# Performance work log

Hardware: AMD Instinct MI355X
Metric: run time of the kernel (lower is better)

Reference implementation:

```python
import jax, jax.numpy as jnp
import numpy as np

N, E, G = 50000, 800000, 128
IN_C, H, EDGE_D, NUM_CLASSES, NUM_LAYERS = 26, 64, 3, 2, 4

def _p(k, shape):
    return jax.random.normal(k, shape, dtype=jnp.float32) * 0.05

def setup_inputs() -> dict:
    key = jax.random.key(0)
    ks = list(jax.random.split(key, 32))
    x = jax.random.normal(ks[0], (N, IN_C), dtype=jnp.float32)
    pos = jax.random.normal(ks[1], (N, 3), dtype=jnp.float32)
    row = jax.random.randint(ks[2], (E,), 0, N, dtype=jnp.int32)
    # avoid self-loops so dist > 0 (norm is non-differentiable at 0)
    off = jax.random.randint(ks[3], (E,), 1, N, dtype=jnp.int32)
    col = (row + off) % N
    edge_index = jnp.stack([row, col], axis=0)
    edge_attr = jax.random.normal(ks[4], (E, EDGE_D), dtype=jnp.float32)
    batch = jnp.sort(jax.random.randint(ks[5], (N,), 0, G, dtype=jnp.int32))
    inp = dict(x=x, pos=pos, edge_index=edge_index, edge_attr=edge_attr, batch=batch)
    inp['proj_W'] = _p(ks[6], (IN_C, H)); inp['proj_b'] = jnp.zeros((H,), jnp.float32)
    inp['msg_W1'] = _p(ks[7], (NUM_LAYERS, 2*H + 1 + EDGE_D, H)); inp['msg_b1'] = jnp.zeros((NUM_LAYERS, H), jnp.float32)
    inp['msg_W2'] = _p(ks[8], (NUM_LAYERS, H, H)); inp['msg_b2'] = jnp.zeros((NUM_LAYERS, H), jnp.float32)
    inp['node_W1'] = _p(ks[9], (NUM_LAYERS, 2*H, H)); inp['node_b1'] = jnp.zeros((NUM_LAYERS, H), jnp.float32)
    inp['node_W2'] = _p(ks[10], (NUM_LAYERS, H, H)); inp['node_b2'] = jnp.zeros((NUM_LAYERS, H), jnp.float32)
    inp['coord_W1'] = _p(ks[11], (NUM_LAYERS - 1, H, H)); inp['coord_b1'] = jnp.zeros((NUM_LAYERS - 1, H), jnp.float32)
    inp['coord_W2'] = _p(ks[12], (NUM_LAYERS - 1, H, 1)); inp['coord_b2'] = jnp.zeros((NUM_LAYERS - 1, 1), jnp.float32)
    inp['cls_W1'] = _p(ks[13], (2*H, H)); inp['cls_b1'] = jnp.zeros((H,), jnp.float32)
    inp['cls_W2'] = _p(ks[14], (H, NUM_CLASSES)); inp['cls_b2'] = jnp.zeros((NUM_CLASSES,), jnp.float32)
    return inp

def _egnn_forward(x, pos, edge_index, edge_attr, batch,
                  proj_W, proj_b, msg_W1, msg_b1, msg_W2, msg_b2,
                  node_W1, node_b1, node_W2, node_b2,
                  coord_W1, coord_b1, coord_W2, coord_b2,
                  cls_W1, cls_b1, cls_W2, cls_b2):
    silu = jax.nn.silu
    row, col = edge_index[0], edge_index[1]
    h = x @ proj_W + proj_b  # [N,H]
    for i in range(NUM_LAYERS):
        diff = pos[row] - pos[col]                      # [E,3]
        dist = jnp.linalg.norm(diff, axis=-1, keepdims=True)  # [E,1]
        msg_in = jnp.concatenate([h[row], h[col], dist, edge_attr], axis=-1)  # [E,2H+1+edge_dim]
        msg = silu(silu(msg_in @ msg_W1[i] + msg_b1[i]) @ msg_W2[i] + msg_b2[i])  # [E,H]
        agg = jax.ops.segment_sum(msg, row, num_segments=N)  # [N,H]
        h_new = silu(jnp.concatenate([h, agg], axis=-1) @ node_W1[i] + node_b1[i]) @ node_W2[i] + node_b2[i]
        h = h + h_new  # residual; dropout is identity at eval
        if i < NUM_LAYERS - 1:
            w = silu(msg @ coord_W1[i] + coord_b1[i]) @ coord_W2[i] + coord_b2[i]  # [E,1]
            pos = pos + jax.ops.segment_sum(diff * w, row, num_segments=N)
    # mean_max pooling over graphs
    sums = jax.ops.segment_sum(h, batch, num_segments=G)
    counts = jax.ops.segment_sum(jnp.ones((h.shape[0],), h.dtype), batch, num_segments=G)
    mean = sums / jnp.maximum(counts, 1.0)[:, None]
    mx = jax.ops.segment_max(h, batch, num_segments=G)
    pooled = jnp.concatenate([mean, mx], axis=-1)  # [G,2H]
    return jax.nn.relu(pooled @ cls_W1 + cls_b1) @ cls_W2 + cls_b2  # [G,num_classes]

def reference(x, pos, edge_index, edge_attr, batch,
              proj_W, proj_b, msg_W1, msg_b1, msg_W2, msg_b2,
              node_W1, node_b1, node_W2, node_b2,
              coord_W1, coord_b1, coord_W2, coord_b2,
              cls_W1, cls_b1, cls_W2, cls_b2):
    return _egnn_forward(x, pos, edge_index, edge_attr, batch,
                         proj_W, proj_b, msg_W1, msg_b1, msg_W2, msg_b2,
                         node_W1, node_b1, node_W2, node_b2,
                         coord_W1, coord_b1, coord_W2, coord_b2,
                         cls_W1, cls_b1, cls_W2, cls_b2)
```

## Files before the change

### kernel.cpp

```cpp
#include <hip/hip_runtime.h>
#include <math.h>


typedef __attribute__((ext_vector_type(8))) short bshort8;
typedef __attribute__((ext_vector_type(4))) float f32x4;
typedef unsigned short ushort;
typedef unsigned int uint;

__device__ __forceinline__ float silu_f(float x)
{
  return x * __builtin_amdgcn_rcpf(1.0f + __expf(-x));
}

__device__ __forceinline__ void bf16_split(float x, ushort& h, ushort& l)
{
  uint bx = __float_as_uint(x);
  ushort hb = (ushort)(bx >> 16);
  float hf = __uint_as_float((uint)hb << 16);
  float r = x - hf;
  l = (ushort)(__float_as_uint(r) >> 16);
  h = hb;
}

#define ROW_FMA(acc, scal, rowptr)                                                   \
  {                                                                                  \
    const float4* _w = (const float4*)(rowptr);                                      \
    _Pragma("unroll") for (int _j = 0; _j < 16; _j++)                                \
    {                                                                                \
      float4 _wv = _w[_j];                                                           \
      acc[4 * _j + 0] += (scal) * _wv.x;                                             \
      acc[4 * _j + 1] += (scal) * _wv.y;                                             \
      acc[4 * _j + 2] += (scal) * _wv.z;                                             \
      acc[4 * _j + 3] += (scal) * _wv.w;                                             \
    }                                                                                \
  }

__global__ __launch_bounds__(256) void proj_kernel(
    const float* __restrict__ x, const float* __restrict__ W, const float* __restrict__ b,
    float* __restrict__ h, int N)
{
  __shared__ float sW[26 * 64];
  __shared__ float sb[64];
  for (int i = threadIdx.x; i < 26 * 64; i += 256) sW[i] = W[i];
  if (threadIdx.x < 64) sb[threadIdx.x] = b[threadIdx.x];
  __syncthreads();
  int n = blockIdx.x * 256 + threadIdx.x;
  if (n >= N) return;
  float acc[64];
#pragma unroll
  for (int j = 0; j < 64; j++) acc[j] = sb[j];
#pragma unroll
  for (int k = 0; k < 26; k++) {
    float xk = x[(size_t)n * 26 + k];
    ROW_FMA(acc, xk, sW + k * 64);
  }
  float4* h4 = (float4*)(h + (size_t)n * 64);
#pragma unroll
  for (int j4 = 0; j4 < 16; j4++) {
    float4 v;
    v.x = acc[4 * j4 + 0]; v.y = acc[4 * j4 + 1]; v.z = acc[4 * j4 + 2]; v.w = acc[4 * j4 + 3];
    h4[j4] = v;
  }
}

#define EB 128

__device__ __forceinline__ bshort8 lds_frag(const ushort* base, int edge, int kb)
{
  int byte = edge * 128 + kb * 2;
  byte ^= (edge & 7) << 4;
  return *(const bshort8*)((const char*)base + byte);
}

__device__ __forceinline__ void stage_tile_f32(
    const float* __restrict__ src, int n0, int N, ushort* sHi, ushort* sLo, int t)
{
#pragma unroll
  for (int p = 0; p < 4; p++) {
    int nl = p * 32 + (t >> 3);
    int ks = t & 7;
    int n = n0 + nl;
    int base = nl * 128 + ks * 16;
    int swz = (nl & 7) << 4;
    if (n < N) {
      const float4* sp = (const float4*)(src + (size_t)n * 64) + ks * 2;
      float4 a0 = sp[0], a1 = sp[1];
      float va[8] = {a0.x, a0.y, a0.z, a0.w, a1.x, a1.y, a1.z, a1.w};
      ushort hh[8], ll[8];
#pragma unroll
      for (int kk = 0; kk < 8; kk++) bf16_split(va[kk], hh[kk], ll[kk]);
      uint4 hv, lv;
      hv.x = (uint)hh[0] | ((uint)hh[1] << 16);
      hv.y = (uint)hh[2] | ((uint)hh[3] << 16);
      hv.z = (uint)hh[4] | ((uint)hh[5] << 16);
      hv.w = (uint)hh[6] | ((uint)hh[7] << 16);
      lv.x = (uint)ll[0] | ((uint)ll[1] << 16);
      lv.y = (uint)ll[2] | ((uint)ll[3] << 16);
      lv.z = (uint)ll[4] | ((uint)ll[5] << 16);
      lv.w = (uint)ll[6] | ((uint)ll[7] << 16);
      *(uint4*)((char*)sHi + (base ^ swz)) = hv;
      *(uint4*)((char*)sLo + (base ^ swz)) = lv;
    } else {
      uint4 z; z.x = 0; z.y = 0; z.z = 0; z.w = 0;
      *(uint4*)((char*)sHi + (base ^ swz)) = z;
      *(uint4*)((char*)sLo + (base ^ swz)) = z;
    }
  }
}

#define PANEL_MFMA(accv, bhp, blp, sHi, sLo)                                         \
  {                                                                                  \
    bshort8 wh0 = *(const bshort8*)(bhp);                                            \
    bshort8 wh1 = *(const bshort8*)((bhp) + 32);                                     \
    bshort8 wl0 = *(const bshort8*)(blp);                                            \
    bshort8 wl1 = *(const bshort8*)((blp) + 32);                                     \
    _Pragma("unroll") for (int et = 0; et < 8; et++)                                 \
    {                                                                                \
      int nd = et * 16 + lane16;                                                     \
      bshort8 ah0 = lds_frag(sHi, nd, kq * 8);                                       \
      bshort8 ah1 = lds_frag(sHi, nd, 32 + kq * 8);                                  \
      bshort8 al0 = lds_frag(sLo, nd, kq * 8);                                       \
      bshort8 al1 = lds_frag(sLo, nd, 32 + kq * 8);                                  \
      f32x4 a = accv[et];                                                            \
      a = __builtin_amdgcn_mfma_f32_16x16x32_bf16(wh0, ah0, a, 0, 0, 0);             \
      a = __builtin_amdgcn_mfma_f32_16x16x32_bf16(wh1, ah1, a, 0, 0, 0);             \
      a = __builtin_amdgcn_mfma_f32_16x16x32_bf16(wh0, al0, a, 0, 0, 0);             \
      a = __builtin_amdgcn_mfma_f32_16x16x32_bf16(wh1, al1, a, 0, 0, 0);             \
      a = __builtin_amdgcn_mfma_f32_16x16x32_bf16(wl0, ah0, a, 0, 0, 0);             \
      a = __builtin_amdgcn_mfma_f32_16x16x32_bf16(wl1, ah1, a, 0, 0, 0);             \
      accv[et] = a;                                                                  \
    }                                                                                \
  }

__global__ __launch_bounds__(256) void premul_mfma_kernel(
    const float* __restrict__ h, const ushort* __restrict__ pqh, const ushort* __restrict__ pql,
    float* __restrict__ P, float* __restrict__ Q, int N)
{
  __shared__ ushort sAhi[EB * 64];
  __shared__ ushort sAlo[EB * 64];
  int t = threadIdx.x;
  int n0 = blockIdx.x * EB;
  stage_tile_f32(h, n0, N, sAhi, sAlo, t);
  __syncthreads();

  int l = t & 63, wv = t >> 6, lane16 = l & 15, kq = l >> 4;
  int col = wv * 16 + kq * 4;

  f32x4 acc[8];
#pragma unroll
  for (int et = 0; et < 8; et++) { f32x4 z = {0.f, 0.f, 0.f, 0.f}; acc[et] = z; }
  {
    const ushort* bh = pqh + (wv * 16 + lane16) * 64 + kq * 8;
    const ushort* bl = pql + (wv * 16 + lane16) * 64 + kq * 8;
    PANEL_MFMA(acc, bh, bl, sAhi, sAlo);
  }
#pragma unroll
  for (int et = 0; et < 8; et++) {
    int n = n0 + et * 16 + lane16;
    if (n < N) {
      float4 v; v.x = acc[et][0]; v.y = acc[et][1]; v.z = acc[et][2]; v.w = acc[et][3];
      *(float4*)(P + (size_t)n * 64 + col) = v;
    }
  }
#pragma unroll
  for (int et = 0; et < 8; et++) { f32x4 z = {0.f, 0.f, 0.f, 0.f}; acc[et] = z; }
  {
    const ushort* bh = pqh + 4096 + (wv * 16 + lane16) * 64 + kq * 8;
    const ushort* bl = pql + 4096 + (wv * 16 + lane16) * 64 + kq * 8;
    PANEL_MFMA(acc, bh, bl, sAhi, sAlo);
  }
#pragma unroll
  for (int et = 0; et < 8; et++) {
    int n = n0 + et * 16 + lane16;
    if (n < N) {
      float4 v; v.x = acc[et][0]; v.y = acc[et][1]; v.z = acc[et][2]; v.w = acc[et][3];
      *(float4*)(Q + (size_t)n * 64 + col) = v;
    }
  }
}

template <int PREMUL>
__global__ __launch_bounds__(256) void node_mfma_kernel(
    float* __restrict__ h, const float* __restrict__ agg,
    const ushort* __restrict__ n1h, const ushort* __restrict__ n1l,
    const float* __restrict__ b1,
    const ushort* __restrict__ n2h, const ushort* __restrict__ n2l,
    const float* __restrict__ b2,
    const ushort* __restrict__ pqh, const ushort* __restrict__ pql,
    float* __restrict__ P, float* __restrict__ Q, int N)
{
  __shared__ ushort sAhi[EB * 64];
  __shared__ ushort sAlo[EB * 64];
  __shared__ float sb1v[64], sb2v[64];
  int t = threadIdx.x;
  int n0 = blockIdx.x * EB;
  if (t < 64) { sb1v[t] = b1[t]; sb2v[t] = b2[t]; }

  stage_tile_f32(h, n0, N, sAhi, sAlo, t);
  __syncthreads();

  int l = t & 63, wv = t >> 6, lane16 = l & 15, kq = l >> 4;
  int col = wv * 16 + kq * 4;

  f32x4 acc[8];
#pragma unroll
  for (int et = 0; et < 8; et++) { f32x4 z = {0.f, 0.f, 0.f, 0.f}; acc[et] = z; }
  {
    const ushort* bh = n1h + (wv * 16 + lane16) * 128 + kq * 8;
    const ushort* bl = n1l + (wv * 16 + lane16) * 128 + kq * 8;
    PANEL_MFMA(acc, bh, bl, sAhi, sAlo);
  }
  __syncthreads();
  stage_tile_f32(agg, n0, N, sAhi, sAlo, t);
  __syncthreads();
  {
    const ushort* bh = n1h + (wv * 16 + lane16) * 128 + 64 + kq * 8;
    const ushort* bl = n1l + (wv * 16 + lane16) * 128 + 64 + kq * 8;
    PANEL_MFMA(acc, bh, bl, sAhi, sAlo);
  }
  __syncthreads();

  {
    float b1r[4];
#pragma unroll
    for (int r = 0; r < 4; r++) b1r[r] = sb1v[col + r];
#pragma unroll
    for (int et = 0; et < 8; et++) {
      int nd = et * 16 + lane16;
      ushort uh[4], ul[4];
#pragma unroll
      for (int r = 0; r < 4; r++) {
        float uv = silu_f(acc[et][r] + b1r[r]);
        bf16_split(uv, uh[r], ul[r]);
      }
      int byte = (nd * 128 + col * 2) ^ ((nd & 7) << 4);
      uint2 hv, lv;
      hv.x = (uint)uh[0] | ((uint)uh[1] << 16);
      hv.y = (uint)uh[2] | ((uint)uh[3] << 16);
      lv.x = (uint)ul[0] | ((uint)ul[1] << 16);
      lv.y = (uint)ul[2] | ((uint)ul[3] << 16);
      *(uint2*)((char*)sAhi + byte) = hv;
      *(uint2*)((char*)sAlo + byte) = lv;
    }
  }
  __syncthreads();

#pragma unroll
  for (int et = 0; et < 8; et++) { f32x4 z = {0.f, 0.f, 0.f, 0.f}; acc[et] = z; }
  {
    const ushort* bh = n2h + (wv * 16 + lane16) * 64 + kq * 8;
    const ushort* bl = n2l + (wv * 16 + lane16) * 64 + kq * 8;
    PANEL_MFMA(acc, bh, bl, sAhi, sAlo);
  }
  uint2 hnh[8], hnl[8];
  {
    float b2r[4];
#pragma unroll
    for (int r = 0; r < 4; r++) b2r[r] = sb2v[col + r];
#pragma unroll
    for (int et = 0; et < 8; et++) {
      int n = n0 + et * 16 + lane16;
      float hn[4];
      if (n < N) {
        float4 hv = *(float4*)(h + (size_t)n * 64 + col);
        hn[0] = hv.x + acc[et][0] + b2r[0];
        hn[1] = hv.y + acc[et][1] + b2r[1];
        hn[2] = hv.z + acc[et][2] + b2r[2];
        hn[3] = hv.w + acc[et][3] + b2r[3];
        float4 sv; sv.x = hn[0]; sv.y = hn[1]; sv.z = hn[2]; sv.w = hn[3];
        *(float4*)(h + (size_t)n * 64 + col) = sv;
      } else {
        hn[0] = hn[1] = hn[2] = hn[3] = 0.f;
      }
      if (PREMUL) {
        ushort sh[4], sl[4];
#pragma unroll
        for (int r = 0; r < 4; r++) bf16_split(hn[r], sh[r], sl[r]);
        hnh[et].x = (uint)sh[0] | ((uint)sh[1] << 16);
        hnh[et].y = (uint)sh[2] | ((uint)sh[3] << 16);
        hnl[et].x = (uint)sl[0] | ((uint)sl[1] << 16);
        hnl[et].y = (uint)sl[2] | ((uint)sl[3] << 16);
      }
    }
  }

  if (PREMUL) {
    __syncthreads();
#pragma unroll
    for (int et = 0; et < 8; et++) {
      int nd = et * 16 + lane16;
      int byte = (nd * 128 + col * 2) ^ ((nd & 7) << 4);
      *(uint2*)((char*)sAhi + byte) = hnh[et];
      *(uint2*)((char*)sAlo + byte) = hnl[et];
    }
    __syncthreads();
#pragma unroll
    for (int et = 0; et < 8; et++) { f32x4 z = {0.f, 0.f, 0.f, 0.f}; acc[et] = z; }
    {
      const ushort* bh = pqh + (wv * 16 + lane16) * 64 + kq * 8;
      const ushort* bl = pql + (wv * 16 + lane16) * 64 + kq * 8;
      PANEL_MFMA(acc, bh, bl, sAhi, sAlo);
    }
#pragma unroll
    for (int et = 0; et < 8; et++) {
      int n = n0 + et * 16 + lane16;
      if (n < N) {
        float4 v; v.x = acc[et][0]; v.y = acc[et][1]; v.z = acc[et][2]; v.w = acc[et][3];
        *(float4*)(P + (size_t)n * 64 + col) = v;
      }
    }
#pragma unroll
    for (int et = 0; et < 8; et++) { f32x4 z = {0.f, 0.f, 0.f, 0.f}; acc[et] = z; }
    {
      const ushort* bh = pqh + 4096 + (wv * 16 + lane16) * 64 + kq * 8;
      const ushort* bl = pql + 4096 + (wv * 16 + lane16) * 64 + kq * 8;
      PANEL_MFMA(acc, bh, bl, sAhi, sAlo);
    }
#pragma unroll
    for (int et = 0; et < 8; et++) {
      int n = n0 + et * 16 + lane16;
      if (n < N) {
        float4 v; v.x = acc[et][0]; v.y = acc[et][1]; v.z = acc[et][2]; v.w = acc[et][3];
        *(float4*)(Q + (size_t)n * 64 + col) = v;
      }
    }
  }
}

__global__ __launch_bounds__(256) void hist_kernel(
    const int* __restrict__ row, int* __restrict__ cnt, int E)
{
  int e = blockIdx.x * 256 + threadIdx.x;
  if (e < E) atomicAdd(&cnt[row[e]], 1);
}

__global__ __launch_bounds__(1024) void scan_kernel(
    const int* __restrict__ cnt, int* __restrict__ rowptr, int* __restrict__ cursor, int N, int E)
{
  __shared__ int part[1024];
  int t = threadIdx.x;
  int chunk = (N + 1023) >> 10;
  int lo = t * chunk;
  int hi = lo + chunk;
  if (lo > N) lo = N;
  if (hi > N) hi = N;
  int s = 0;
  for (int i = lo; i < hi; i++) s += cnt[i];
  part[t] = s;
  __syncthreads();
  for (int off = 1; off < 1024; off <<= 1) {
    int v = 0;
    if (t >= off) v = part[t - off];
    __syncthreads();
    if (t >= off) part[t] += v;
    __syncthreads();
  }
  int run = part[t] - s;
  for (int i = lo; i < hi; i++) {
    rowptr[i] = run;
    cursor[i] = run;
    run += cnt[i];
  }
  if (t == 0) rowptr[N] = E;
}

__global__ __launch_bounds__(256) void scatter_kernel(
    const int* __restrict__ row, const int* __restrict__ col, const float* __restrict__ eattr,
    int* __restrict__ cursor, int* __restrict__ srow, int* __restrict__ scol,
    float* __restrict__ sea4, int E)
{
  int e = blockIdx.x * 256 + threadIdx.x;
  if (e >= E) return;
  int r = row[e];
  int p = atomicAdd(&cursor[r], 1);
  srow[p] = r;
  scol[p] = col[e];
  float4 v;
  v.x = eattr[(size_t)e * 3 + 0];
  v.y = eattr[(size_t)e * 3 + 1];
  v.z = eattr[(size_t)e * 3 + 2];
  v.w = 0.f;
  ((float4*)sea4)[p] = v;
}

__global__ __launch_bounds__(256) void prep_wt_kernel(
    const float* __restrict__ W2all, const float* __restrict__ C1all,
    ushort* __restrict__ w2h, ushort* __restrict__ w2l,
    ushort* __restrict__ c1h, ushort* __restrict__ c1l)
{
  int idx = blockIdx.x * 256 + threadIdx.x;
  if (idx >= 4 * 4096) return;
  int layer = idx >> 12, rem = idx & 4095;
  int k = rem >> 6, c = rem & 63;
  int oidx = layer * 4096 + c * 64 + k;
  ushort h, l;
  bf16_split(W2all[idx], h, l);
  w2h[oidx] = h; w2l[oidx] = l;
  if (layer < 3) {
    bf16_split(C1all[idx], h, l);
    c1h[oidx] = h; c1l[oidx] = l;
  }
}

__global__ __launch_bounds__(256) void prep_nd_kernel(
    const float* __restrict__ ndW1, const float* __restrict__ ndW2,
    const float* __restrict__ msgW1,
    ushort* __restrict__ n1h, ushort* __restrict__ n1l,
    ushort* __restrict__ n2h, ushort* __restrict__ n2l,
    ushort* __restrict__ pqh, ushort* __restrict__ pql)
{
  int idx = blockIdx.x * 256 + threadIdx.x;
  if (idx < 4 * 8192) {
    int i = idx >> 13, rem = idx & 8191;
    int k = rem >> 6, c = rem & 63;
    ushort h, l;
    bf16_split(ndW1[idx], h, l);
    int o = i * 8192 + c * 128 + k;
    n1h[o] = h; n1l[o] = l;
  }
  if (idx < 4 * 4096) {
    int i = idx >> 12, rem = idx & 4095;
    int k = rem >> 6, c = rem & 63;
    ushort h, l;
    bf16_split(ndW2[idx], h, l);
    int o = i * 4096 + c * 64 + k;
    n2h[o] = h; n2l[o] = l;
  }
  if (idx < 4 * 8192) {
    int i = idx >> 13, rem = idx & 8191;
    int k = rem >> 6, c = rem & 63;
    ushort h, l;
    bf16_split(msgW1[(size_t)i * 132 * 64 + k * 64 + c], h, l);
    int o = i * 8192 + (k >> 6) * 4096 + c * 64 + (k & 63);
    pqh[o] = h; pql[o] = l;
  }
}

template <int COORD>
__global__ __launch_bounds__(256) void edge_fused_kernel(
    const int* __restrict__ srow, const int* __restrict__ scol, const int* __restrict__ rowptr,
    const float* __restrict__ posr, float* __restrict__ posw,
    const float* __restrict__ sea4,
    const float* __restrict__ P, const float* __restrict__ Q,
    const float* __restrict__ W1t, const float* __restrict__ b1,
    const ushort* __restrict__ w2h, const ushort* __restrict__ w2l,
    const float* __restrict__ b2,
    const ushort* __restrict__ c1h, const ushort* __restrict__ c1l,
    const float* __restrict__ cb1, const float* __restrict__ cW2,
    const float* __restrict__ cb2,
    float* __restrict__ agg, int E)
{
  __shared__ ushort sUhi[EB * 64];
  __shared__ ushort sUlo[EB * 64];
  __shared__ float sW1t[4 * 64];
  __shared__ float sb1v[64], sb2v[64];
  __shared__ float sDiff[3][EB];
  __shared__ float sWe[EB];
  __shared__ int sShare[COORD ? EB * 4 : EB];
  __shared__ float scb1v[COORD ? 64 : 1];
  __shared__ float scW2v[COORD ? 64 : 1];
  __shared__ int sSlotCnt[2];
  __shared__ int sSlotStart[EB + 2];
  __shared__ int sSlotRowF[EB];

  int* s_srow = sShare;
  float* sPart = (float*)sShare;

  int t = threadIdx.x;
  sW1t[t] = W1t[t];
  if (t < 64) { sb1v[t] = b1[t]; sb2v[t] = b2[t]; }
  if (COORD && t >= 64 && t < 128) { scb1v[t - 64] = cb1[t - 64]; scW2v[t - 64] = cW2[t - 64]; }
  __syncthreads();

  int e0 = blockIdx.x * EB;
  int nE = E - e0; if (nE > EB) nE = EB;

#pragma unroll
  for (int p = 0; p < 4; p++) {
    int eloc = p * 32 + (t >> 3);
    int ks = t & 7;
    int e = e0 + eloc;
    int base = eloc * 128 + ks * 16;
    int swz = (eloc & 7) << 4;
    if (e < E) {
      int r = srow[e];
      int c = scol[e];
      float prx = posr[(size_t)r * 3 + 0], pry = posr[(size_t)r * 3 + 1],
            prz = posr[(size_t)r * 3 + 2];
      float pcx = posr[(size_t)c * 3 + 0], pcy = posr[(size_t)c * 3 + 1],
            pcz = posr[(size_t)c * 3 + 2];
      float dx = prx - pcx, dy = pry - pcy, dz = prz - pcz;
      float dist = sqrtf(dx * dx + dy * dy + dz * dz);
      if (ks == 0) {
        s_srow[eloc] = r;
        sDiff[0][eloc] = dx; sDiff[1][eloc] = dy; sDiff[2][eloc] = dz;
      }
      float4 ea = ((const float4*)sea4)[e];
      const float4* P4p = (const float4*)(P + (size_t)r * 64) + ks * 2;
      const float4* Q4p = (const float4*)(Q + (size_t)c * 64) + ks * 2;
      float4 a0 = P4p[0], a1 = P4p[1];
      float4 q0 = Q4p[0], q1 = Q4p[1];
      float pa[8] = {a0.x, a0.y, a0.z, a0.w, a1.x, a1.y, a1.z, a1.w};
      float qa[8] = {q0.x, q0.y, q0.z, q0.w, q1.x, q1.y, q1.z, q1.w};
      ushort hh[8], ll[8];
#pragma unroll
      for (int kk = 0; kk < 8; kk++) {
        int k = ks * 8 + kk;
        float val = pa[kk] + qa[kk] + sb1v[k] + dist * sW1t[k] + ea.x * sW1t[64 + k] +
                    ea.y * sW1t[128 + k] + ea.z * sW1t[192 + k];
        float uv = silu_f(val);
        bf16_split(uv, hh[kk], ll[kk]);
      }
      uint4 hv, lv;
      hv.x = (uint)hh[0] | ((uint)hh[1] << 16);
      hv.y = (uint)hh[2] | ((uint)hh[3] << 16);
      hv.z = (uint)hh[4] | ((uint)hh[5] << 16);
      hv.w = (uint)hh[6] | ((uint)hh[7] << 16);
      lv.x = (uint)ll[0] | ((uint)ll[1] << 16);
      lv.y = (uint)ll[2] | ((uint)ll[3] << 16);
      lv.z = (uint)ll[4] | ((uint)ll[5] << 16);
      lv.w = (uint)ll[6] | ((uint)ll[7] << 16);
      *(uint4*)((char*)sUhi + (base ^ swz)) = hv;
      *(uint4*)((char*)sUlo + (base ^ swz)) = lv;
    } else {
      uint4 z; z.x = 0; z.y = 0; z.z = 0; z.w = 0;
      *(uint4*)((char*)sUhi + (base ^ swz)) = z;
      *(uint4*)((char*)sUlo + (base ^ swz)) = z;
    }
  }
  __syncthreads();

  bool isstart = false;
  int pre = 0;
  if (t < 128) {
    int le = t;
    isstart = (le < nE) && (le == 0 || s_srow[le] != s_srow[le - 1]);
    unsigned long long m = __ballot(isstart ? 1 : 0);
    int lane = t & 63;
    pre = __popcll(m & ((lane == 0) ? 0ull : ((~0ull) >> (64 - lane))));
    if (lane == 0) sSlotCnt[t >> 6] = __popcll(m);
  }
  __syncthreads();
  if (t < 128 && isstart) {
    int le = t;
    int slot = ((t >> 6) ? sSlotCnt[0] : 0) + pre;
    int row = s_srow[le];
    sSlotStart[slot] = le;
    int rs = rowptr[row], re = rowptr[row + 1];
    int interior = (rs >= e0 && re <= e0 + nE) ? 1 : 0;
    sSlotRowF[slot] = row | (interior << 30);
  }
  if (t == 0) sSlotStart[sSlotCnt[0] + sSlotCnt[1]] = nE;

  int l = t & 63;
  int wv = t >> 6;
  int lane16 = l & 15;
  int kq = l >> 4;

  {
    const ushort* bhp = w2h + (wv * 16 + lane16) * 64 + kq * 8;
    const ushort* blp = w2l + (wv * 16 + lane16) * 64 + kq * 8;
    bshort8 wh0 = *(const bshort8*)(bhp);
    bshort8 wh1 = *(const bshort8*)(bhp + 32);
    bshort8 wl0 = *(const bshort8*)(blp);
    bshort8 wl1 = *(const bshort8*)(blp + 32);

    f32x4 acc[8];
#pragma unroll
    for (int et = 0; et < 8; et++) {
      int edge = et * 16 + lane16;
      bshort8 uh0 = lds_frag(sUhi, edge, kq * 8);
      bshort8 uh1 = lds_frag(sUhi, edge, 32 + kq * 8);
      bshort8 ul0 = lds_frag(sUlo, edge, kq * 8);
      bshort8 ul1 = lds_frag(sUlo, edge, 32 + kq * 8);
      f32x4 a = {0.f, 0.f, 0.f, 0.f};
      a = __builtin_amdgcn_mfma_f32_16x16x32_bf16(wh0, uh0, a, 0, 0, 0);
      a = __builtin_amdgcn_mfma_f32_16x16x32_bf16(wh1, uh1, a, 0, 0, 0);
      a = __builtin_amdgcn_mfma_f32_16x16x32_bf16(wh0, ul0, a, 0, 0, 0);
      a = __builtin_amdgcn_mfma_f32_16x16x32_bf16(wh1, ul1, a, 0, 0, 0);
      a = __builtin_amdgcn_mfma_f32_16x16x32_bf16(wl0, uh0, a, 0, 0, 0);
      a = __builtin_amdgcn_mfma_f32_16x16x32_bf16(wl1, uh1, a, 0, 0, 0);
      acc[et] = a;
    }
    __syncthreads();

    float b2r[4];
#pragma unroll
    for (int r = 0; r < 4; r++) b2r[r] = sb2v[wv * 16 + kq * 4 + r];
#pragma unroll
    for (int et = 0; et < 8; et++) {
      int edge = et * 16 + lane16;
      ushort mh[4], ml[4];
#pragma unroll
      for (int r = 0; r < 4; r++) {
        float mv = silu_f(acc[et][r] + b2r[r]);
        bf16_split(mv, mh[r], ml[r]);
      }
      int byte = (edge * 128 + (wv * 16 + kq * 4) * 2) ^ ((edge & 7) << 4);
      uint2 hv, lv;
      hv.x = (uint)mh[0] | ((uint)mh[1] << 16);
      hv.y = (uint)mh[2] | ((uint)mh[3] << 16);
      lv.x = (uint)ml[0] | ((uint)ml[1] << 16);
      lv.y = (uint)ml[2] | ((uint)ml[3] << 16);
      *(uint2*)((char*)sUhi + byte) = hv;
      *(uint2*)((char*)sUlo + byte) = lv;
    }
  }
  __syncthreads();

  if (COORD) {
    const ushort* chp = c1h + (wv * 16 + lane16) * 64 + kq * 8;
    const ushort* clp = c1l + (wv * 16 + lane16) * 64 + kq * 8;
    bshort8 ch0 = *(const bshort8*)(chp);
    bshort8 ch1 = *(const bshort8*)(chp + 32);
    bshort8 cl0 = *(const bshort8*)(clp);
    bshort8 cl1 = *(const bshort8*)(clp + 32);
    float cb1r[4], cw2r[4];
#pragma unroll
    for (int r = 0; r < 4; r++) {
      cb1r[r] = scb1v[wv * 16 + kq * 4 + r];
      cw2r[r] = scW2v[wv * 16 + kq * 4 + r];
    }
#pragma unroll
    for (int et = 0; et < 8; et++) {
      int edge = et * 16 + lane16;
      bshort8 mh0 = lds_frag(sUhi, edge, kq * 8);
      bshort8 mh1 = lds_frag(sUhi, edge, 32 + kq * 8);
      f32x4 a = {0.f, 0.f, 0.f, 0.f};
      a = __builtin_amdgcn_mfma_f32_16x16x32_bf16(ch0, mh0, a, 0, 0, 0);
      a = __builtin_amdgcn_mfma_f32_16x16x32_bf16(ch1, mh1, a, 0, 0, 0);
      a = __builtin_amdgcn_mfma_f32_16x16x32_bf16(cl0, mh0, a, 0, 0, 0);
      a = __builtin_amdgcn_mfma_f32_16x16x32_bf16(cl1, mh1, a, 0, 0, 0);
      float pr = 0.f;
#pragma unroll
      for (int r = 0; r < 4; r++) pr += silu_f(a[r] + cb1r[r]) * cw2r[r];
      pr += __shfl_xor(pr, 16);
      pr += __shfl_xor(pr, 32);
      if (kq == 0) sPart[edge * 4 + wv] = pr;
    }
  }
  __syncthreads();
  if (COORD) {
    if (t >= 128) {
      int e = t - 128;
      sWe[e] = sPart[4 * e + 0] + sPart[4 * e + 1] + sPart[4 * e + 2] + sPart[4 * e + 3] + cb2[0];
    }
  }
  __syncthreads();

  int nslots = sSlotCnt[0] + sSlotCnt[1];
  for (int task = t; task < (nslots << 5); task += 256) {
    int s = task >> 5, cp = task & 31;
    int a = sSlotStart[s], b = sSlotStart[s + 1];
    float acc0 = 0.f, acc1 = 0.f;
    for (int le = a; le < b; le++) {
      int byte = (le * 128 + cp * 4) ^ ((le & 7) << 4);
      uint hv = *(const uint*)((const char*)sUhi + byte);
      uint lv = *(const uint*)((const char*)sUlo + byte);
      acc0 += __uint_as_float(hv << 16) + __uint_as_float(lv << 16);
      acc1 += __uint_as_float(hv & 0xffff0000u) + __uint_as_float(lv & 0xffff0000u);
    }
    int rowf = sSlotRowF[s];
    int row = rowf & 0x3fffffff;
    float* ap = agg + (size_t)row * 64 + 2 * cp;
    if (rowf & (1 << 30)) {
      ap[0] = acc0; ap[1] = acc1;
    } else {
      atomicAdd(ap, acc0);
      atomicAdd(ap + 1, acc1);
    }
  }
  if (COORD) {
    for (int task = t; task < (nslots << 2); task += 256) {
      int s = task >> 2, d = task & 3;
      if (d < 3) {
        int a = sSlotStart[s], b = sSlotStart[s + 1];
        float acc = 0.f;
        for (int le = a; le < b; le++) acc += sDiff[d][le] * sWe[le];
        int row = sSlotRowF[s] & 0x3fffffff;
        atomicAdd(&posw[(size_t)row * 3 + d], acc);
      }
    }
  }
}

__device__ __forceinline__ int lbound(const int* __restrict__ a, int n, int v)
{
  int lo = 0, hi = n;
  while (lo < hi) {
    int mid = (lo + hi) >> 1;
    if (a[mid] < v) lo = mid + 1;
    else hi = mid;
  }
  return lo;
}

__global__ __launch_bounds__(256) void pool_cls_kernel(
    const float* __restrict__ h, const int* __restrict__ batch, int N,
    const float* __restrict__ W1, const float* __restrict__ b1,
    const float* __restrict__ W2, const float* __restrict__ b2, float* __restrict__ out)
{
  int g = blockIdx.x;
  int start = lbound(batch, N, g);
  int end = lbound(batch, N, g + 1);
  int j = threadIdx.x & 63;
  int grp = threadIdx.x >> 6;
  float s = 0.f, mx = -INFINITY;
  for (int n = start + grp; n < end; n += 4) {
    float v = h[(size_t)n * 64 + j];
    s += v;
    mx = fmaxf(mx, v);
  }
  __shared__ float ssum[4][64];
  __shared__ float smax[4][64];
  __shared__ float pooled[128];
  __shared__ float su[64];
  ssum[grp][j] = s;
  smax[grp][j] = mx;
  __syncthreads();
  if (grp == 0) {
    float S = ssum[0][j] + ssum[1][j] + ssum[2][j] + ssum[3][j];
    float M = fmaxf(fmaxf(smax[0][j], smax[1][j]), fmaxf(smax[2][j], smax[3][j]));
    float cnt = (float)(end - start);
    pooled[j] = S / fmaxf(cnt, 1.0f);
    pooled[64 + j] = M;
  }
  __syncthreads();
  if (threadIdx.x < 64) {
    float a = b1[j];
#pragma unroll
    for (int k = 0; k < 128; k++) a += pooled[k] * W1[k * 64 + j];
    su[j] = fmaxf(a, 0.f);
  }
  __syncthreads();
  if (threadIdx.x < 2) {
    float a = b2[threadIdx.x];
#pragma unroll
    for (int k = 0; k < 64; k++) a += su[k] * W2[k * 2 + threadIdx.x];
    out[g * 2 + threadIdx.x] = a;
  }
}

extern "C" void kernel_launch(void* const* d_in, const int* in_sizes, int n_in,
                              void* d_out, int out_size, void* d_ws, size_t ws_size,
                              hipStream_t stream)
{
  const float* x = (const float*)d_in[0];
  const float* pos = (const float*)d_in[1];
  const int* ei = (const int*)d_in[2];
  const float* eattr = (const float*)d_in[3];
  const int* batch = (const int*)d_in[4];
  const float* projW = (const float*)d_in[5];
  const float* projb = (const float*)d_in[6];
  const float* msgW1 = (const float*)d_in[7];
  const float* msgb1 = (const float*)d_in[8];
  const float* msgW2 = (const float*)d_in[9];
  const float* msgb2 = (const float*)d_in[10];
  const float* ndW1 = (const float*)d_in[11];
  const float* ndb1 = (const float*)d_in[12];
  const float* ndW2 = (const float*)d_in[13];
  const float* ndb2 = (const float*)d_in[14];
  const float* cdW1 = (const float*)d_in[15];
  const float* cdb1 = (const float*)d_in[16];
  const float* cdW2 = (const float*)d_in[17];
  const float* cdb2 = (const float*)d_in[18];
  const float* clsW1 = (const float*)d_in[19];
  const float* clsb1 = (const float*)d_in[20];
  const float* clsW2 = (const float*)d_in[21];
  const float* clsb2 = (const float*)d_in[22];

  int N = in_sizes[4];
  int E = in_sizes[3] / 3;
  const int* rowp = ei;
  const int* colp = ei + E;

  char* wsb = (char*)d_ws;
  size_t off = 0;
  auto alloc = [&](size_t bytes) {
    size_t o = off;
    off = (off + bytes + 255) & ~(size_t)255;
    return o;
  };
  size_t nh = (size_t)N * 64 * sizeof(float);
  size_t o_h = alloc(nh);
  size_t o_P = alloc(nh);
  size_t o_Q = alloc(nh);
  size_t o_agg = alloc(nh);
  size_t o_posA = alloc((size_t)N * 3 * sizeof(float));
  size_t o_posB = alloc((size_t)N * 3 * sizeof(float));
  size_t o_cnt = alloc((size_t)N * sizeof(int));
  size_t o_rowptr = alloc(((size_t)N + 1) * sizeof(int));
  size_t o_cursor = alloc((size_t)N * sizeof(int));
  size_t o_srow = alloc((size_t)E * sizeof(int));
  size_t o_scol = alloc((size_t)E * sizeof(int));
  size_t o_sea4 = alloc((size_t)E * 4 * sizeof(float));
  size_t o_w2h = alloc(4 * 4096 * sizeof(ushort));
  size_t o_w2l = alloc(4 * 4096 * sizeof(ushort));
  size_t o_c1h = alloc(4 * 4096 * sizeof(ushort));
  size_t o_c1l = alloc(4 * 4096 * sizeof(ushort));
  size_t o_n1h = alloc(4 * 8192 * sizeof(ushort));
  size_t o_n1l = alloc(4 * 8192 * sizeof(ushort));
  size_t o_n2h = alloc(4 * 4096 * sizeof(ushort));
  size_t o_n2l = alloc(4 * 4096 * sizeof(ushort));
  size_t o_pqh = alloc(4 * 8192 * sizeof(ushort));
  size_t o_pql = alloc(4 * 8192 * sizeof(ushort));
  size_t csr_end = off;

  float* h = (float*)(wsb + o_h);
  float* Pb = (float*)(wsb + o_P);
  float* Qb = (float*)(wsb + o_Q);
  float* agg = (float*)(wsb + o_agg);
  float* posA = (float*)(wsb + o_posA);
  float* posB = (float*)(wsb + o_posB);

  int nb_nodes = (N + 255) / 256;
  int nb_edges = (E + 255) / 256;
  int nb_tiled = (N + EB - 1) / EB;
  int G = out_size / 2;

  proj_kernel<<<nb_nodes, 256, 0, stream>>>(x, projW, projb, h, N);

  const float* pr[4] = {pos, posA, posB, posA};
  float* pw[4] = {posA, posB, posA, nullptr};

  bool use_sorted = (csr_end <= ws_size);

  if (use_sorted) {
    int* cnt = (int*)(wsb + o_cnt);
    int* rowptr = (int*)(wsb + o_rowptr);
    int* cursor = (int*)(wsb + o_cursor);
    int* srow = (int*)(wsb + o_srow);
    int* scol = (int*)(wsb + o_scol);
    float* sea4 = (float*)(wsb + o_sea4);
    ushort* w2h = (ushort*)(wsb + o_w2h);
    ushort* w2l = (ushort*)(wsb + o_w2l);
    ushort* c1h = (ushort*)(wsb + o_c1h);
    ushort* c1l = (ushort*)(wsb + o_c1l);
    ushort* n1h = (ushort*)(wsb + o_n1h);
    ushort* n1l = (ushort*)(wsb + o_n1l);
    ushort* n2h = (ushort*)(wsb + o_n2h);
    ushort* n2l = (ushort*)(wsb + o_n2l);
    ushort* pqh = (ushort*)(wsb + o_pqh);
    ushort* pql = (ushort*)(wsb + o_pql);

    hipMemsetAsync(cnt, 0, (size_t)N * sizeof(int), stream);
    hist_kernel<<<nb_edges, 256, 0, stream>>>(rowp, cnt, E);
    scan_kernel<<<1, 1024, 0, stream>>>(cnt, rowptr, cursor, N, E);
    scatter_kernel<<<nb_edges, 256, 0, stream>>>(rowp, colp, eattr, cursor, srow, scol, sea4, E);
    prep_wt_kernel<<<64, 256, 0, stream>>>(msgW2, cdW1, w2h, w2l, c1h, c1l);
    prep_nd_kernel<<<128, 256, 0, stream>>>(ndW1, ndW2, msgW1, n1h, n1l, n2h, n2l, pqh, pql);

    premul_mfma_kernel<<<nb_tiled, 256, 0, stream>>>(h, pqh, pql, Pb, Qb, N);

    int nb_fused = (E + EB - 1) / EB;
    for (int i = 0; i < 4; i++) {
      hipMemsetAsync(agg, 0, nh, stream);
      if (i < 3) {
        hipMemcpyAsync(pw[i], pr[i], (size_t)N * 3 * sizeof(float), hipMemcpyDeviceToDevice,
                       stream);
        edge_fused_kernel<1><<<nb_fused, 256, 0, stream>>>(
            srow, scol, rowptr, pr[i], pw[i], sea4, Pb, Qb,
            msgW1 + (size_t)i * 132 * 64 + 128 * 64, msgb1 + i * 64,
            w2h + (size_t)i * 4096, w2l + (size_t)i * 4096, msgb2 + i * 64,
            c1h + (size_t)i * 4096, c1l + (size_t)i * 4096,
            cdb1 + i * 64, cdW2 + i * 64, cdb2 + i, agg, E);
        node_mfma_kernel<1><<<nb_tiled, 256, 0, stream>>>(
            h, agg, n1h + (size_t)i * 8192, n1l + (size_t)i * 8192, ndb1 + i * 64,
            n2h + (size_t)i * 4096, n2l + (size_t)i * 4096, ndb2 + i * 64,
            pqh + (size_t)(i + 1) * 8192, pql + (size_t)(i + 1) * 8192, Pb, Qb, N);
      } else {
        edge_fused_kernel<0><<<nb_fused, 256, 0, stream>>>(
            srow, scol, rowptr, pr[i], nullptr, sea4, Pb, Qb,
            msgW1 + (size_t)i * 132 * 64 + 128 * 64, msgb1 + i * 64,
            w2h + (size_t)i * 4096, w2l + (size_t)i * 4096, msgb2 + i * 64,
            nullptr, nullptr, nullptr, nullptr, nullptr, agg, E);
        node_mfma_kernel<0><<<nb_tiled, 256, 0, stream>>>(
            h, agg, n1h + (size_t)i * 8192, n1l + (size_t)i * 8192, ndb1 + i * 64,
            n2h + (size_t)i * 4096, n2l + (size_t)i * 4096, ndb2 + i * 64,
            nullptr, nullptr, nullptr, nullptr, N);
      }
    }
  }

  pool_cls_kernel<<<G, 256, 0, stream>>>(h, batch, N, clsW1, clsb1, clsW2, clsb2, (float*)d_out);
}
```

Before: 796.1 us.

## Overlap coord MLP MFMA with message scatter via warp specialization

In the coordinate-update layers, waves 2-3 now compute the coord MLP for all four column groups, two each, while waves 0-1 run the message aggregation and atomic scatter to agg. The two phases used to run one after the other across all 256 threads. This is meant to hide atomic and LDS latency behind MFMA work and to drop one barrier. In exchange, each half does twice the work per wave, so the two sides may end up imbalanced.

```diff
diff --git a/kernel.cpp b/kernel.cpp
--- a/kernel.cpp
+++ b/kernel.cpp
@@ -608,69 +608,73 @@
   }
   __syncthreads();
 
+  int nslots = sSlotCnt[0] + sSlotCnt[1];
+
   if (COORD) {
-    const ushort* chp = c1h + (wv * 16 + lane16) * 64 + kq * 8;
-    const ushort* clp = c1l + (wv * 16 + lane16) * 64 + kq * 8;
-    bshort8 ch0 = *(const bshort8*)(chp);
-    bshort8 ch1 = *(const bshort8*)(chp + 32);
-    bshort8 cl0 = *(const bshort8*)(clp);
-    bshort8 cl1 = *(const bshort8*)(clp + 32);
-    float cb1r[4], cw2r[4];
-#pragma unroll
-    for (int r = 0; r < 4; r++) {
-      cb1r[r] = scb1v[wv * 16 + kq * 4 + r];
-      cw2r[r] = scW2v[wv * 16 + kq * 4 + r];
-    }
-#pragma unroll
-    for (int et = 0; et < 8; et++) {
-      int edge = et * 16 + lane16;
-      bshort8 mh0 = lds_frag(sUhi, edge, kq * 8);
-      bshort8 mh1 = lds_frag(sUhi, edge, 32 + kq * 8);
-      f32x4 a = {0.f, 0.f, 0.f, 0.f};
-      a = __builtin_amdgcn_mfma_f32_16x16x32_bf16(ch0, mh0, a, 0, 0, 0);
-      a = __builtin_amdgcn_mfma_f32_16x16x32_bf16(ch1, mh1, a, 0, 0, 0);
-      a = __builtin_amdgcn_mfma_f32_16x16x32_bf16(cl0, mh0, a, 0, 0, 0);
-      a = __builtin_amdgcn_mfma_f32_16x16x32_bf16(cl1, mh1, a, 0, 0, 0);
-      float pr = 0.f;
-#pragma unroll
-      for (int r = 0; r < 4; r++) pr += silu_f(a[r] + cb1r[r]) * cw2r[r];
-      pr += __shfl_xor(pr, 16);
-      pr += __shfl_xor(pr, 32);
-      if (kq == 0) sPart[edge * 4 + wv] = pr;
-    }
-  }
-  __syncthreads();
-  if (COORD) {
-    if (t >= 128) {
-      int e = t - 128;
+    if (wv >= 2) {
+#pragma unroll
+      for (int cg2 = 0; cg2 < 2; cg2++) {
+        int colg = (wv - 2) * 2 + cg2;
+        int colb = colg * 16;
+        const ushort* chp = c1h + (colb + lane16) * 64 + kq * 8;
+        const ushort* clp = c1l + (colb + lane16) * 64 + kq * 8;
+        bshort8 ch0 = *(const bshort8*)(chp);
+        bshort8 ch1 = *(const bshort8*)(chp + 32);
+        bshort8 cl0 = *(const bshort8*)(clp);
+        bshort8 cl1 = *(const bshort8*)(clp + 32);
+        float cb1r[4], cw2r[4];
+#pragma unroll
+        for (int r = 0; r < 4; r++) {
+          cb1r[r] = scb1v[colb + kq * 4 + r];
+          cw2r[r] = scW2v[colb + kq * 4 + r];
+        }
+#pragma unroll
+        for (int et = 0; et < 8; et++) {
+          int edge = et * 16 + lane16;
+          bshort8 mh0 = lds_frag(sUhi, edge, kq * 8);
+          bshort8 mh1 = lds_frag(sUhi, edge, 32 + kq * 8);
+          f32x4 a = {0.f, 0.f, 0.f, 0.f};
+          a = __builtin_amdgcn_mfma_f32_16x16x32_bf16(ch0, mh0, a, 0, 0, 0);
+          a = __builtin_amdgcn_mfma_f32_16x16x32_bf16(ch1, mh1, a, 0, 0, 0);
+          a = __builtin_amdgcn_mfma_f32_16x16x32_bf16(cl0, mh0, a, 0, 0, 0);
+          a = __builtin_amdgcn_mfma_f32_16x16x32_bf16(cl1, mh1, a, 0, 0, 0);
+          float pr = 0.f;
+#pragma unroll
+          for (int r = 0; r < 4; r++) pr += silu_f(a[r] + cb1r[r]) * cw2r[r];
+          pr += __shfl_xor(pr, 16);
+          pr += __shfl_xor(pr, 32);
+          if (kq == 0) sPart[edge * 4 + colg] = pr;
+        }
+      }
+    } else {
+      for (int task = t; task < (nslots << 5); task += 128) {
+        int s = task >> 5, cp = task & 31;
+        int a = sSlotStart[s], b = sSlotStart[s + 1];
+        float acc0 = 0.f, acc1 = 0.f;
+        for (int le = a; le < b; le++) {
+          int byte = (le * 128 + cp * 4) ^ ((le & 7) << 4);
+          uint hv = *(const uint*)((const char*)sUhi + byte);
+          uint lv = *(const uint*)((const char*)sUlo + byte);
+          acc0 += __uint_as_float(hv << 16) + __uint_as_float(lv << 16);
+          acc1 += __uint_as_float(hv & 0xffff0000u) + __uint_as_float(lv & 0xffff0000u);
+        }
+        int rowf = sSlotRowF[s];
+        int row = rowf & 0x3fffffff;
+        float* ap = agg + (size_t)row * 64 + 2 * cp;
+        if (rowf & (1 << 30)) {
+          ap[0] = acc0; ap[1] = acc1;
+        } else {
+          atomicAdd(ap, acc0);
+          atomicAdd(ap + 1, acc1);
+        }
+      }
+    }
+    __syncthreads();
+    if (t < 128) {
+      int e = t;
       sWe[e] = sPart[4 * e + 0] + sPart[4 * e + 1] + sPart[4 * e + 2] + sPart[4 * e + 3] + cb2[0];
     }
-  }
-  __syncthreads();
-
-  int nslots = sSlotCnt[0] + sSlotCnt[1];
-  for (int task = t; task < (nslots << 5); task += 256) {
-    int s = task >> 5, cp = task & 31;
-    int a = sSlotStart[s], b = sSlotStart[s + 1];
-    float acc0 = 0.f, acc1 = 0.f;
-    for (int le = a; le < b; le++) {
-      int byte = (le * 128 + cp * 4) ^ ((le & 7) << 4);
-      uint hv = *(const uint*)((const char*)sUhi + byte);
-      uint lv = *(const uint*)((const char*)sUlo + byte);
-      acc0 += __uint_as_float(hv << 16) + __uint_as_float(lv << 16);
-      acc1 += __uint_as_float(hv & 0xffff0000u) + __uint_as_float(lv & 0xffff0000u);
-    }
-    int rowf = sSlotRowF[s];
-    int row = rowf & 0x3fffffff;
-    float* ap = agg + (size_t)row * 64 + 2 * cp;
-    if (rowf & (1 << 30)) {
-      ap[0] = acc0; ap[1] = acc1;
-    } else {
-      atomicAdd(ap, acc0);
-      atomicAdd(ap + 1, acc1);
-    }
-  }
-  if (COORD) {
+    __syncthreads();
     for (int task = t; task < (nslots << 2); task += 256) {
       int s = task >> 2, d = task & 3;
       if (d < 3) {
@@ -679,6 +683,28 @@
         for (int le = a; le < b; le++) acc += sDiff[d][le] * sWe[le];
         int row = sSlotRowF[s] & 0x3fffffff;
         atomicAdd(&posw[(size_t)row * 3 + d], acc);
+      }
+    }
+  } else {
+    for (int task = t; task < (nslots << 5); task += 256) {
+      int s = task >> 5, cp = task & 31;
+      int a = sSlotStart[s], b = sSlotStart[s + 1];
+      float acc0 = 0.f, acc1 = 0.f;
+      for (int le = a; le < b; le++) {
+        int byte = (le * 128 + cp * 4) ^ ((le & 7) << 4);
+        uint hv = *(const uint*)((const char*)sUhi + byte);
+        uint lv = *(const uint*)((const char*)sUlo + byte);
+        acc0 += __uint_as_float(hv << 16) + __uint_as_float(lv << 16);
+        acc1 += __uint_as_float(hv & 0xffff0000u) + __uint_as_float(lv & 0xffff0000u);
+      }
+      int rowf = sSlotRowF[s];
+      int row = rowf & 0x3fffffff;
+      float* ap = agg + (size_t)row * 64 + 2 * cp;
+      if (rowf & (1 << 30)) {
+        ap[0] = acc0; ap[1] = acc1;
+      } else {
+        atomicAdd(ap, acc0);
+        atomicAdd(ap + 1, acc1);
       }
     }
   }
```

New measurement: 858.9 us. 1.08x slower.
